# Kernel optimization log

Hardware: AMD Instinct MI355X
Metric: run time of the kernel (lower is better)

Reference implementation:

```python
import jax, jax.numpy as jnp
import numpy as np

SIZE = 768
INNER = 64

def setup_inputs() -> dict:
    key = jax.random.key(0)
    ks = jax.random.split(key, 7)
    emb_input = jax.random.normal(ks[0], (8, 2048, SIZE), dtype=jnp.float32)
    s = 1.0 / np.sqrt(SIZE)
    Wq = jax.random.normal(ks[1], (INNER, SIZE), dtype=jnp.float32) * s
    bq = jax.random.normal(ks[2], (INNER,), dtype=jnp.float32) * 0.01
    Wk = jax.random.normal(ks[3], (INNER, SIZE), dtype=jnp.float32) * s
    bk = jax.random.normal(ks[4], (INNER,), dtype=jnp.float32) * 0.01
    Wv = jax.random.normal(ks[5], (INNER, SIZE), dtype=jnp.float32) * s
    bv = jax.random.normal(ks[6], (INNER,), dtype=jnp.float32) * 0.01
    return {"emb_input": emb_input, "Wq": Wq, "bq": bq, "Wk": Wk, "bk": bk, "Wv": Wv, "bv": bv}

def reference(emb_input, Wq, bq, Wk, bk, Wv, bv):
    # q,k,v: (B,S,inner)
    q = jnp.einsum('bse,ie->bsi', emb_input, Wq) + bq
    k = jnp.einsum('bse,ie->bsi', emb_input, Wk) + bk
    v = jnp.einsum('bse,ie->bsi', emb_input, Wv) + bv
    # NOTE: original scales by sqrt(emb_size), not sqrt(inner_size)
    scale = 1.0 / np.sqrt(SIZE).astype(np.float32)
    attn = jnp.einsum('bqi,bki->bqk', q, k) * scale  # (B,S,S)
    attn = jax.nn.softmax(attn, axis=2)
    # attn @ v, same math as original broadcast-mul-sum but as a matmul
    return jnp.einsum('bqk,bki->bqi', attn, v)
```

## Files before the change

### kernel.cpp

```cpp
#include <hip/hip_runtime.h>
#include <hip/hip_bf16.h>
#include <math.h>

#define B_  8
#define S_  2048
#define E_  768
#define I_  64

typedef __attribute__((ext_vector_type(4))) float f32x4;
typedef __attribute__((ext_vector_type(8))) short short8;
typedef __attribute__((ext_vector_type(4))) short short4v;

static __device__ __forceinline__ short bf16_of(float x) {
    unsigned u = __builtin_bit_cast(unsigned, x);
    u += 0x7fffu + ((u >> 16) & 1u);
    return (short)(u >> 16);
}

static __device__ __forceinline__ unsigned pk2(float lo, float hi) {
    __hip_bfloat162 h = __float22bfloat162_rn(float2{lo, hi});
    unsigned u; __builtin_memcpy(&u, &h, 4);
    return u;
}
static __device__ __forceinline__ short8 pk8(f32x4 a, f32x4 b) {
    union { unsigned u[4]; short8 s; } r;
    r.u[0] = pk2(a[0], a[1]); r.u[1] = pk2(a[2], a[3]);
    r.u[2] = pk2(b[0], b[1]); r.u[3] = pk2(b[2], b[3]);
    return r.s;
}

typedef __attribute__((address_space(1))) const void gv_t;
typedef __attribute__((address_space(3))) void lv_t;
static __device__ __forceinline__ void gload16(const void* g, void* l) {
    __builtin_amdgcn_global_load_lds((gv_t*)g, (lv_t*)l, 16, 0, 0);
}

#define BARRIER()   asm volatile("s_barrier" ::: "memory")
#define VMCNT(n)    asm volatile("s_waitcnt vmcnt(" #n ")" ::: "memory")

__global__ void wconv(const float* __restrict__ Wq, const float* __restrict__ bq,
                      const float* __restrict__ Wk, const float* __restrict__ bk,
                      const float* __restrict__ Wv, const float* __restrict__ bv,
                      short* __restrict__ Wb, float* __restrict__ bb, float qscale) {
    int r = blockIdx.x;
    const float* src; const float* bsrc; float sc;
    if (r < 64)       { src = Wq + r * E_;         bsrc = bq + r;         sc = qscale; }
    else if (r < 128) { src = Wk + (r - 64) * E_;  bsrc = bk + (r - 64);  sc = 1.0f; }
    else              { src = Wv + (r - 128) * E_; bsrc = bv + (r - 128); sc = 1.0f; }
    for (int j = threadIdx.x; j < E_; j += blockDim.x)
        Wb[r * E_ + j] = bf16_of(src[j] * sc);
    if (threadIdx.x == 0) bb[r] = bsrc[0] * sc;
}

__global__ __launch_bounds__(256) void qkv_proj(
    const float* __restrict__ emb, const short* __restrict__ Wb,
    const float* __restrict__ bb,
    short* __restrict__ qb, short* __restrict__ kb, short* __restrict__ vT)
{
    __shared__ float Af[2][32][64];
    __shared__ short Wf[2][192][64];

    const int tid = threadIdx.x, w = tid >> 6, l = tid & 63;
    const int lr = l & 15, rg = l >> 4;
    const int sm = w & 1, sc = w >> 1;
    const int m0 = blockIdx.x * 32;

    f32x4 acc[6];
#pragma unroll
    for (int t = 0; t < 6; ++t) acc[t] = (f32x4){0.f, 0.f, 0.f, 0.f};

    auto STAGE = [&](int ks, int d) {
        char* ab = (char*)&Af[d][0][0] + w * 2048;
#pragma unroll
        for (int i = 0; i < 2; ++i) {
            int r = w * 8 + i * 4 + (l >> 4);
            const float* src = emb + (size_t)(m0 + r) * E_ + ks * 64 + (((l & 15) ^ (r & 15)) << 2);
            gload16(src, ab + i * 1024);
        }
        char* wb2 = (char*)&Wf[d][0][0] + w * 6144;
#pragma unroll
        for (int i = 0; i < 6; ++i) {
            int r = w * 48 + i * 8 + (l >> 3);
            const short* src = Wb + (size_t)r * E_ + ks * 64 + (((l & 7) ^ (r & 7)) << 3);
            gload16(src, wb2 + i * 1024);
        }
    };

    STAGE(0, 0);
    STAGE(1, 1);

    for (int ks = 0; ks < 12; ++ks) {
        const int cur = ks & 1;
        if (ks == 11) { VMCNT(0); } else { VMCNT(8); }
        BARRIER();
#pragma unroll
        for (int h = 0; h < 2; ++h) {
            const int r = sm * 16 + lr;
            const int s0 = (h * 8 + rg * 2) ^ lr;
            const int s1 = (h * 8 + rg * 2 + 1) ^ lr;
            f32x4 a0 = *(const f32x4*)&Af[cur][r][s0 * 4];
            f32x4 a1 = *(const f32x4*)&Af[cur][r][s1 * 4];
            short8 af = pk8(a0, a1);
#pragma unroll
            for (int tt = 0; tt < 6; ++tt) {
                int rw = (sc * 6 + tt) * 16 + lr;
                short8 wf = *(const short8*)&Wf[cur][rw][((h * 4 + rg) ^ (lr & 7)) << 3];
                acc[tt] = __builtin_amdgcn_mfma_f32_16x16x32_bf16(af, wf, acc[tt], 0, 0, 0);
            }
        }
        BARRIER();
        if (ks + 2 < 12) STAGE(ks + 2, cur);
    }

#pragma unroll
    for (int tt = 0; tt < 6; ++tt) {
        int col = sc * 96 + tt * 16 + lr;
        float bias = bb[col];
        int row = m0 + sm * 16 + rg * 4;
        if (col < 64) {
#pragma unroll
            for (int j = 0; j < 4; ++j)
                qb[(size_t)(row + j) * 64 + col] = bf16_of(acc[tt][j] + bias);
        } else if (col < 128) {
#pragma unroll
            for (int j = 0; j < 4; ++j)
                kb[(size_t)(row + j) * 64 + (col - 64)] = bf16_of(acc[tt][j] + bias);
        } else {
            short4v pv;
#pragma unroll
            for (int j = 0; j < 4; ++j) pv[j] = bf16_of(acc[tt][j] + bias);
            int b = row >> 11, s = row & 2047;
            *(short4v*)&vT[((size_t)b * 64 + (col - 128)) * S_ + s] = pv;
        }
    }
}

__global__ __launch_bounds__(512) void flash_attn(
    const short* __restrict__ qb, const short* __restrict__ kb,
    const short* __restrict__ vT, float* __restrict__ out)
{
    __shared__ __align__(16) char smem[81920];
    short (*Kb)[2][32][64] = (short(*)[2][32][64])(smem);
    short (*Vb)[2][64][32] = (short(*)[2][64][32])(smem + 32768);
    uint2 (*pbuf)[32][8]   = (uint2(*)[32][8])  (smem + 65536);
    float* mpart  = (float*)smem;
    float* rspart = (float*)(smem + 49152);

    const int tid = threadIdx.x, w = tid >> 6, l = tid & 63;
    const int lr = l & 15, rg = l >> 4;
    const int g = w & 1, c = w >> 1;
    const int batch = blockIdx.x & 7;
    const int qt = blockIdx.x >> 3;
    const int qloc0 = qt * 64 + g * 32;

    const short* kbB = kb + (size_t)batch * S_ * 64;
    const short* vTB = vT + (size_t)batch * 64 * S_;

    const int swk = ((l & 7) ^ (l >> 3)) << 3;
    const int swv = (((l & 3) ^ ((l >> 3) & 3)) << 3);
    auto STAGE = [&](int ks, int d) {
        const int k0 = c * 512 + ks * 32;
#pragma unroll
        for (int i = 0; i < 2; ++i) {
            const int rloc = g * 16 + i * 8;
            gload16(kbB + (size_t)(k0 + rloc + (l >> 3)) * 64 + swk,
                    (char*)&Kb[c][d][rloc][0]);
            const int dloc = g * 32 + i * 16;
            gload16(vTB + (size_t)(dloc + (l >> 2)) * S_ + k0 + swv,
                    (char*)&Vb[c][d][dloc][0]);
        }
    };

    short8 aq[2][2];
#pragma unroll
    for (int mg = 0; mg < 2; ++mg)
#pragma unroll
        for (int h = 0; h < 2; ++h)
            aq[mg][h] = *(const short8*)(qb + (size_t)(batch * S_ + qloc0 + mg * 16 + lr) * 64 + h * 32 + rg * 8);

    f32x4 acc[2][4];
    float rs[2] = {0.f, 0.f};
#pragma unroll
    for (int mg = 0; mg < 2; ++mg)
#pragma unroll
        for (int n = 0; n < 4; ++n) acc[mg][n] = (f32x4){0.f, 0.f, 0.f, 0.f};

    uint2* pwr[2][4];
    const uint2* prd[2];
#pragma unroll
    for (int mg = 0; mg < 2; ++mg) {
#pragma unroll
        for (int t = 0; t < 2; ++t) {
            pwr[mg][t * 2 + 0] = &pbuf[w][mg * 16 + lr][(t * 4 + rg) ^ ((lr & 3) << 1)];
            pwr[mg][t * 2 + 1] = pwr[mg][t * 2 + 0];
        }
        prd[mg] = &pbuf[w][mg * 16 + lr][2 * (rg ^ (lr & 3))];
    }

    STAGE(0, 0);
    STAGE(1, 1);

    for (int ks = 0; ks < 16; ++ks) {
        const int cur = ks & 1;
        if (ks == 15) { VMCNT(0); } else { VMCNT(4); }
        BARRIER();

        f32x4 s2[2][2];
#pragma unroll
        for (int t = 0; t < 2; ++t) {
            const int rk = t * 16 + lr;
            short8 kf0 = *(const short8*)&Kb[c][cur][rk][((0 * 4 + rg) ^ (lr & 7)) << 3];
            short8 kf1 = *(const short8*)&Kb[c][cur][rk][((1 * 4 + rg) ^ (lr & 7)) << 3];
#pragma unroll
            for (int mg = 0; mg < 2; ++mg) {
                f32x4 z = (f32x4){0.f, 0.f, 0.f, 0.f};
                z = __builtin_amdgcn_mfma_f32_16x16x32_bf16(kf0, aq[mg][0], z, 0, 0, 0);
                s2[mg][t] = __builtin_amdgcn_mfma_f32_16x16x32_bf16(kf1, aq[mg][1], z, 0, 0, 0);
            }
        }
#pragma unroll
        for (int mg = 0; mg < 2; ++mg)
#pragma unroll
            for (int t = 0; t < 2; ++t) {
                float p0 = __builtin_amdgcn_exp2f(s2[mg][t][0]);
                float p1 = __builtin_amdgcn_exp2f(s2[mg][t][1]);
                float p2 = __builtin_amdgcn_exp2f(s2[mg][t][2]);
                float p3 = __builtin_amdgcn_exp2f(s2[mg][t][3]);
                rs[mg] += (p0 + p1) + (p2 + p3);
                *pwr[mg][t * 2] = uint2{pk2(p0, p1), pk2(p2, p3)};
            }
        short8 pa[2];
#pragma unroll
        for (int mg = 0; mg < 2; ++mg) pa[mg] = *(const short8*)prd[mg];
#pragma unroll
        for (int n = 0; n < 4; ++n) {
            short8 vf = *(const short8*)&Vb[c][cur][n * 16 + lr][(rg ^ ((lr >> 1) & 3)) * 8];
#pragma unroll
            for (int mg = 0; mg < 2; ++mg)
                acc[mg][n] = __builtin_amdgcn_mfma_f32_16x16x32_bf16(pa[mg], vf, acc[mg][n], 0, 0, 0);
        }

        BARRIER();
        if (ks + 2 < 16) STAGE(ks + 2, cur);
    }

#pragma unroll
    for (int mg = 0; mg < 2; ++mg) {
        rs[mg] += __shfl_xor(rs[mg], 16, 64);
        rs[mg] += __shfl_xor(rs[mg], 32, 64);
    }

    if (c != 0) {
        const int base = ((c - 1) * 2 + g) * 2048 + l * 32;
#pragma unroll
        for (int mg = 0; mg < 2; ++mg) {
#pragma unroll
            for (int n = 0; n < 4; ++n)
#pragma unroll
                for (int j = 0; j < 4; ++j)
                    mpart[base + mg * 16 + n * 4 + j] = acc[mg][n][j];
            if (l < 16) rspart[((c - 1) * 2 + g) * 32 + mg * 16 + l] = rs[mg];
        }
    }
    __syncthreads();
    if (c == 0) {
#pragma unroll
        for (int mg = 0; mg < 2; ++mg) {
            const int qrow = batch * S_ + qloc0 + mg * 16 + rg * 4;
#pragma unroll
            for (int j = 0; j < 4; ++j) {
                const int qj = rg * 4 + j;
                float tot = __shfl(rs[mg], qj, 64);
#pragma unroll
                for (int cc = 0; cc < 3; ++cc)
                    tot += rspart[(cc * 2 + g) * 32 + mg * 16 + qj];
                float inv = 1.0f / tot;
                float* orow = out + (size_t)(qrow + j) * 64;
#pragma unroll
                for (int n = 0; n < 4; ++n) {
                    float v = acc[mg][n][j];
#pragma unroll
                    for (int cc = 0; cc < 3; ++cc)
                        v += mpart[(cc * 2 + g) * 2048 + l * 32 + mg * 16 + n * 4 + j];
                    orow[n * 16 + lr] = v * inv;
                }
            }
        }
    }
}

extern "C" void kernel_launch(void* const* d_in, const int* in_sizes, int n_in,
                              void* d_out, int out_size, void* d_ws, size_t ws_size,
                              hipStream_t stream) {
    const float* emb = (const float*)d_in[0];
    const float* Wq  = (const float*)d_in[1];
    const float* bq  = (const float*)d_in[2];
    const float* Wk  = (const float*)d_in[3];
    const float* bk  = (const float*)d_in[4];
    const float* Wv  = (const float*)d_in[5];
    const float* bv  = (const float*)d_in[6];
    float* out = (float*)d_out;

    char* ws = (char*)d_ws;
    short* Wb  = (short*)(ws + 0);
    float* bb  = (float*)(ws + 294912);
    short* qb  = (short*)(ws + 295680);
    short* kb  = (short*)(ws + 295680 + 2097152);
    short* vT  = (short*)(ws + 295680 + 2 * 2097152);

    const float qscale = 1.4426950408889634f / sqrtf((float)E_);

    hipLaunchKernelGGL(wconv, dim3(192), dim3(256), 0, stream,
                       Wq, bq, Wk, bk, Wv, bv, Wb, bb, qscale);
    hipLaunchKernelGGL(qkv_proj, dim3(512), dim3(256), 0, stream,
                       emb, Wb, bb, qb, kb, vT);
    hipLaunchKernelGGL(flash_attn, dim3(256), dim3(512), 0, stream,
                       qb, kb, vT, out);
}
```

Before: 44.86 us.

## Split keys across eight waves per block with per-wave K staging and direct V loads

The attention kernel now uses 32 query rows per block and eight waves, each covering its own 256-key slice, so the grid doubles to 512 blocks. Each wave stages only its own K tiles, which removes the block-wide barriers inside the key loop, and V fragments are read straight from global memory instead of through shared memory. The final reduction merges partial outputs and row sums from eight waves instead of four. The aim is more parallelism and less synchronisation, at the cost of uncoalesced global V reads and a larger cross-wave reduction. The launch-bounds occupancy hint may be unattainable with about 80 KB of shared memory per block.

```diff
diff --git a/kernel.cpp b/kernel.cpp
--- a/kernel.cpp
+++ b/kernel.cpp
@@ -135,40 +135,30 @@
     }
 }
 
-__global__ __launch_bounds__(512) void flash_attn(
+__global__ __launch_bounds__(512, 4) void flash_attn(
     const short* __restrict__ qb, const short* __restrict__ kb,
     const short* __restrict__ vT, float* __restrict__ out)
 {
     __shared__ __align__(16) char smem[81920];
     short (*Kb)[2][32][64] = (short(*)[2][32][64])(smem);
-    short (*Vb)[2][64][32] = (short(*)[2][64][32])(smem + 32768);
-    uint2 (*pbuf)[32][8]   = (uint2(*)[32][8])  (smem + 65536);
-    float* mpart  = (float*)smem;
-    float* rspart = (float*)(smem + 49152);
-
-    const int tid = threadIdx.x, w = tid >> 6, l = tid & 63;
+    uint2 (*pbuf)[32][8]   = (uint2(*)[32][8])(smem + 65536);
+
+    const int tid = threadIdx.x, c = tid >> 6, l = tid & 63;
     const int lr = l & 15, rg = l >> 4;
-    const int g = w & 1, c = w >> 1;
     const int batch = blockIdx.x & 7;
     const int qt = blockIdx.x >> 3;
-    const int qloc0 = qt * 64 + g * 32;
+    const int qloc0 = qt * 32;
 
     const short* kbB = kb + (size_t)batch * S_ * 64;
     const short* vTB = vT + (size_t)batch * 64 * S_;
 
     const int swk = ((l & 7) ^ (l >> 3)) << 3;
-    const int swv = (((l & 3) ^ ((l >> 3) & 3)) << 3);
-    auto STAGE = [&](int ks, int d) {
-        const int k0 = c * 512 + ks * 32;
-#pragma unroll
-        for (int i = 0; i < 2; ++i) {
-            const int rloc = g * 16 + i * 8;
-            gload16(kbB + (size_t)(k0 + rloc + (l >> 3)) * 64 + swk,
-                    (char*)&Kb[c][d][rloc][0]);
-            const int dloc = g * 32 + i * 16;
-            gload16(vTB + (size_t)(dloc + (l >> 2)) * S_ + k0 + swv,
-                    (char*)&Vb[c][d][dloc][0]);
-        }
+    auto STAGE = [&](int ks2, int d) {
+        const int k0 = c * 256 + ks2 * 32;
+        char* kd = (char*)&Kb[c][d][0][0];
+#pragma unroll
+        for (int i = 0; i < 4; ++i)
+            gload16(kbB + (size_t)(k0 + i * 8 + (l >> 3)) * 64 + swk, kd + i * 1024);
     };
 
     short8 aq[2][2];
@@ -185,32 +175,25 @@
 #pragma unroll
         for (int n = 0; n < 4; ++n) acc[mg][n] = (f32x4){0.f, 0.f, 0.f, 0.f};
 
-    uint2* pwr[2][4];
-    const uint2* prd[2];
-#pragma unroll
-    for (int mg = 0; mg < 2; ++mg) {
-#pragma unroll
-        for (int t = 0; t < 2; ++t) {
-            pwr[mg][t * 2 + 0] = &pbuf[w][mg * 16 + lr][(t * 4 + rg) ^ ((lr & 3) << 1)];
-            pwr[mg][t * 2 + 1] = pwr[mg][t * 2 + 0];
-        }
-        prd[mg] = &pbuf[w][mg * 16 + lr][2 * (rg ^ (lr & 3))];
-    }
-
     STAGE(0, 0);
     STAGE(1, 1);
 
-    for (int ks = 0; ks < 16; ++ks) {
+    for (int ks = 0; ks < 8; ++ks) {
         const int cur = ks & 1;
-        if (ks == 15) { VMCNT(0); } else { VMCNT(4); }
-        BARRIER();
+        if (ks == 7) { VMCNT(0); } else { VMCNT(4); }
+
+        const int k0 = c * 256 + ks * 32;
+        short8 vf[4];
+#pragma unroll
+        for (int n = 0; n < 4; ++n)
+            vf[n] = *(const short8*)(vTB + (size_t)(n * 16 + lr) * S_ + k0 + rg * 8);
 
         f32x4 s2[2][2];
 #pragma unroll
         for (int t = 0; t < 2; ++t) {
             const int rk = t * 16 + lr;
-            short8 kf0 = *(const short8*)&Kb[c][cur][rk][((0 * 4 + rg) ^ (lr & 7)) << 3];
-            short8 kf1 = *(const short8*)&Kb[c][cur][rk][((1 * 4 + rg) ^ (lr & 7)) << 3];
+            short8 kf0 = *(const short8*)&Kb[c][cur][rk][((0 + rg) ^ (lr & 7)) << 3];
+            short8 kf1 = *(const short8*)&Kb[c][cur][rk][((4 + rg) ^ (lr & 7)) << 3];
 #pragma unroll
             for (int mg = 0; mg < 2; ++mg) {
                 f32x4 z = (f32x4){0.f, 0.f, 0.f, 0.f};
@@ -227,21 +210,19 @@
                 float p2 = __builtin_amdgcn_exp2f(s2[mg][t][2]);
                 float p3 = __builtin_amdgcn_exp2f(s2[mg][t][3]);
                 rs[mg] += (p0 + p1) + (p2 + p3);
-                *pwr[mg][t * 2] = uint2{pk2(p0, p1), pk2(p2, p3)};
+                pbuf[c][mg * 16 + lr][(t * 4 + rg) ^ (lr & 6)] = uint2{pk2(p0, p1), pk2(p2, p3)};
             }
         short8 pa[2];
 #pragma unroll
-        for (int mg = 0; mg < 2; ++mg) pa[mg] = *(const short8*)prd[mg];
-#pragma unroll
-        for (int n = 0; n < 4; ++n) {
-            short8 vf = *(const short8*)&Vb[c][cur][n * 16 + lr][(rg ^ ((lr >> 1) & 3)) * 8];
+        for (int mg = 0; mg < 2; ++mg)
+            pa[mg] = *(const short8*)&pbuf[c][mg * 16 + lr][(rg * 2) ^ (lr & 6)];
+#pragma unroll
+        for (int n = 0; n < 4; ++n)
 #pragma unroll
             for (int mg = 0; mg < 2; ++mg)
-                acc[mg][n] = __builtin_amdgcn_mfma_f32_16x16x32_bf16(pa[mg], vf, acc[mg][n], 0, 0, 0);
-        }
-
-        BARRIER();
-        if (ks + 2 < 16) STAGE(ks + 2, cur);
+                acc[mg][n] = __builtin_amdgcn_mfma_f32_16x16x32_bf16(pa[mg], vf[n], acc[mg][n], 0, 0, 0);
+
+        if (ks + 2 < 8) STAGE(ks + 2, cur);
     }
 
 #pragma unroll
@@ -251,15 +232,16 @@
     }
 
     if (c != 0) {
-        const int base = ((c - 1) * 2 + g) * 2048 + l * 32;
+        float* mp = (float*)(smem + c * 8192);
+        float* rp = (float*)(smem + 65536 + c * 2048);
 #pragma unroll
         for (int mg = 0; mg < 2; ++mg) {
 #pragma unroll
             for (int n = 0; n < 4; ++n)
 #pragma unroll
                 for (int j = 0; j < 4; ++j)
-                    mpart[base + mg * 16 + n * 4 + j] = acc[mg][n][j];
-            if (l < 16) rspart[((c - 1) * 2 + g) * 32 + mg * 16 + l] = rs[mg];
+                    mp[l * 32 + mg * 16 + n * 4 + j] = acc[mg][n][j];
+            if (l < 16) rp[mg * 16 + l] = rs[mg];
         }
     }
     __syncthreads();
@@ -272,16 +254,16 @@
                 const int qj = rg * 4 + j;
                 float tot = __shfl(rs[mg], qj, 64);
 #pragma unroll
-                for (int cc = 0; cc < 3; ++cc)
-                    tot += rspart[(cc * 2 + g) * 32 + mg * 16 + qj];
+                for (int cc = 1; cc < 8; ++cc)
+                    tot += ((const float*)(smem + 65536 + cc * 2048))[mg * 16 + qj];
                 float inv = 1.0f / tot;
                 float* orow = out + (size_t)(qrow + j) * 64;
 #pragma unroll
                 for (int n = 0; n < 4; ++n) {
                     float v = acc[mg][n][j];
 #pragma unroll
-                    for (int cc = 0; cc < 3; ++cc)
-                        v += mpart[(cc * 2 + g) * 2048 + l * 32 + mg * 16 + n * 4 + j];
+                    for (int cc = 1; cc < 8; ++cc)
+                        v += ((const float*)(smem + cc * 8192))[l * 32 + mg * 16 + n * 4 + j];
                     orow[n * 16 + lr] = v * inv;
                 }
             }
@@ -314,6 +296,6 @@
                        Wq, bq, Wk, bk, Wv, bv, Wb, bb, qscale);
     hipLaunchKernelGGL(qkv_proj, dim3(512), dim3(256), 0, stream,
                        emb, Wb, bb, qb, kb, vT);
-    hipLaunchKernelGGL(flash_attn, dim3(256), dim3(512), 0, stream,
+    hipLaunchKernelGGL(flash_attn, dim3(512), dim3(512), 0, stream,
                        qb, kb, vT, out);
 }
```

After: 50.46 us. 1.12x slower.
